# Kernel tuning notes

Hardware: AMD Instinct MI355X
Metric: run time of the kernel (lower is better)

The kernel has to match this reference:

```python
import jax, jax.numpy as jnp
import numpy as np

B, T, N1, N2, D, H, DH = 8, 4, 1024, 64, 1024, 16, 64
INNER = H * DH
EPS = 1e-5


def layernorm(x, g, b):
    mu = jnp.mean(x, axis=-1, keepdims=True)
    var = jnp.var(x, axis=-1, keepdims=True)
    return (x - mu) * jax.lax.rsqrt(var + EPS) * g + b


def setup_inputs() -> dict:
    key = jax.random.key(0)
    ks = jax.random.split(key, 8)
    s = 0.02
    return {
        "x": jax.random.normal(ks[0], (B, T, N1, D), jnp.float32),
        "latents": jax.random.normal(ks[1], (B, T, N2, D), jnp.float32),
        "gm": jnp.ones((D,), jnp.float32),
        "bm": jnp.zeros((D,), jnp.float32),
        "gl": jnp.ones((D,), jnp.float32),
        "bl": jnp.zeros((D,), jnp.float32),
        "Wq": jax.random.normal(ks[2], (D, INNER), jnp.float32) * s,
        "Wkv": jax.random.normal(ks[3], (D, 2 * INNER), jnp.float32) * s,
        "Wout": jax.random.normal(ks[4], (INNER, D), jnp.float32) * s,
        "Wd1": jax.random.normal(ks[5], (D, D // 4), jnp.float32) * s,
        "bd1": jnp.zeros((D // 4,), jnp.float32),
        "Wd2": jax.random.normal(ks[6], (D // 4, H), jnp.float32) * s,
        "bd2": jnp.zeros((H,), jnp.float32),
    }


def reference(x, latents, gm, bm, gl, bl, Wq, Wkv, Wout, Wd1, bd1, Wd2, bd2):
    b, t, n1, d = x.shape
    n2 = latents.shape[2]
    h, dh = H, DH
    scale = dh ** -0.5

    xn = layernorm(x, gm, bm)
    ln = layernorm(latents, gl, bl)

    # q: (b, h, t, n2, dh)
    q = (ln @ Wq).reshape(b, t, n2, h, dh).transpose(0, 3, 1, 2, 4)
    # kv over image tokens + first latent token -> nk = n1 + 1
    kv_in = jnp.concatenate([xn, ln[:, :, 0:1]], axis=2)
    nk = n1 + 1
    kv = (kv_in @ Wkv).reshape(b, t, nk, 2, h, dh)
    k = kv[:, :, :, 0].transpose(0, 3, 1, 2, 4)  # (b, h, t, nk, dh)
    v = kv[:, :, :, 1].transpose(0, 3, 1, 2, 4)

    sim = jnp.einsum('bhtid,bhtjd->bhtij', q * scale, k)
    sim = sim - jax.lax.stop_gradient(jnp.max(sim, axis=-1, keepdims=True))
    attn = jax.nn.softmax(sim, axis=-1)

    # dynamic per-head weights from mean-pooled (normed) latents: (b, t, h)
    hid = jax.nn.relu(ln.mean(axis=2) @ Wd1 + bd1)
    dw = jax.nn.softmax(hid @ Wd2 + bd2, axis=-1)
    attn = attn * dw.transpose(0, 2, 1)[:, :, :, None, None]  # (b,h,t,1,1)

    out = jnp.einsum('bhtij,bhtjd->bhtid', attn, v)
    out = out.transpose(0, 2, 3, 1, 4).reshape(b, t, n2, h * dh)
    return out @ Wout
```

## Files before the change

kernel.cpp:

```cpp
#include <hip/hip_runtime.h>
#include <cstdint>
#include <cstddef>

constexpr int CB = 8, CT = 4, CN1 = 1024, CN2 = 64, CD = 1024, CH = 16, CDH = 64;
constexpr int CBT = CB * CT;
constexpr int CNK = CN1 + 1;
constexpr int CINNER = CH * CDH;

__device__ __forceinline__ unsigned short f2bf(float f) {
  union { float f; unsigned int u; } v; v.f = f;
  unsigned int u = v.u;
  u += 0x7fffu + ((u >> 16) & 1u);
  return (unsigned short)(u >> 16);
}
__device__ __forceinline__ float blo(unsigned int w) {
  union { unsigned int u; float f; } v; v.u = w << 16; return v.f;
}
__device__ __forceinline__ float bhi(unsigned int w) {
  union { unsigned int u; float f; } v; v.u = w & 0xffff0000u; return v.f;
}

typedef __attribute__((ext_vector_type(8))) short short8;
typedef __attribute__((ext_vector_type(8))) __bf16 bf16x8;
typedef __attribute__((ext_vector_type(4))) float floatx4;

template <typename V>
__device__ __forceinline__ auto mfma_bf16_impl(V a, V b, floatx4 c, int)
    -> decltype(__builtin_amdgcn_mfma_f32_16x16x32_bf16(a, b, c, 0, 0, 0)) {
  return __builtin_amdgcn_mfma_f32_16x16x32_bf16(a, b, c, 0, 0, 0);
}
template <typename V>
__device__ __forceinline__ floatx4 mfma_bf16_impl(V a, V b, floatx4 c, long) {
  return __builtin_amdgcn_mfma_f32_16x16x32_bf16(
      __builtin_bit_cast(bf16x8, a), __builtin_bit_cast(bf16x8, b), c, 0, 0, 0);
}
__device__ __forceinline__ floatx4 mfma_bf16(short8 a, short8 b, floatx4 c) {
  return mfma_bf16_impl(a, b, c, 0);
}

#if __has_builtin(__builtin_amdgcn_global_load_lds)
#define HAS_GLDS 1
__device__ __forceinline__ void glds16(const unsigned short* g, unsigned short* l) {
  __builtin_amdgcn_global_load_lds(
      (const __attribute__((address_space(1))) void*)g,
      (__attribute__((address_space(3))) void*)l, 16, 0, 0);
}
#else
#define HAS_GLDS 0
#endif

__global__ __launch_bounds__(256) void ln_kernel(
    const float* __restrict__ x, const float* __restrict__ g,
    const float* __restrict__ b, unsigned short* __restrict__ obf,
    float* __restrict__ of32) {
  __shared__ float red[8];
  const int row = blockIdx.x, tid = threadIdx.x;
  const float4 xv = ((const float4*)(x + (size_t)row * CD))[tid];
  float s  = xv.x + xv.y + xv.z + xv.w;
  float s2 = xv.x*xv.x + xv.y*xv.y + xv.z*xv.z + xv.w*xv.w;
#pragma unroll
  for (int off = 32; off; off >>= 1) { s += __shfl_xor(s, off); s2 += __shfl_xor(s2, off); }
  if ((tid & 63) == 0) { red[tid >> 6] = s; red[4 + (tid >> 6)] = s2; }
  __syncthreads();
  const float fs  = red[0] + red[1] + red[2] + red[3];
  const float fs2 = red[4] + red[5] + red[6] + red[7];
  const float mean = fs * (1.0f / 1024.0f);
  const float var  = fs2 * (1.0f / 1024.0f) - mean * mean;
  const float rstd = rsqrtf(var + 1e-5f);
  const float4 gv = ((const float4*)g)[tid];
  const float4 bv = ((const float4*)b)[tid];
  float4 y;
  y.x = (xv.x - mean) * rstd * gv.x + bv.x;
  y.y = (xv.y - mean) * rstd * gv.y + bv.y;
  y.z = (xv.z - mean) * rstd * gv.z + bv.z;
  y.w = (xv.w - mean) * rstd * gv.w + bv.w;
  ushort4 o; o.x = f2bf(y.x); o.y = f2bf(y.y); o.z = f2bf(y.z); o.w = f2bf(y.w);
  ((ushort4*)(obf + (size_t)row * CD))[tid] = o;
  if (of32) ((float4*)(of32 + (size_t)row * CD))[tid] = y;
}

__global__ __launch_bounds__(256) void wtrans_kernel(
    const float* __restrict__ W, unsigned short* __restrict__ WT, int K, int N) {
  __shared__ float t[64][65];
  const int n0 = blockIdx.x * 64, k0 = blockIdx.y * 64;
  const int tid = threadIdx.x;
  const int kr = tid >> 4, ns = (tid & 15) * 4;
#pragma unroll
  for (int i = 0; i < 4; ++i) {
    const int k = kr + i * 16;
    const float4 v = *(const float4*)&W[(size_t)(k0 + k) * N + n0 + ns];
    t[k][ns + 0] = v.x; t[k][ns + 1] = v.y; t[k][ns + 2] = v.z; t[k][ns + 3] = v.w;
  }
  __syncthreads();
  const int n = tid >> 2, ks = (tid & 3) * 16;
#pragma unroll
  for (int c = 0; c < 4; ++c) {
    ushort4 o;
    o.x = f2bf(t[ks + c * 4 + 0][n]);
    o.y = f2bf(t[ks + c * 4 + 1][n]);
    o.z = f2bf(t[ks + c * 4 + 2][n]);
    o.w = f2bf(t[ks + c * 4 + 3][n]);
    *(ushort4*)&WT[(size_t)(n0 + n) * K + k0 + ks + c * 4] = o;
  }
}

template <bool A_KV, bool C_BF16>
__global__ __launch_bounds__(256) void gemm128_kernel(
    const unsigned short* __restrict__ A, const unsigned short* __restrict__ xn,
    const unsigned short* __restrict__ lnb, const unsigned short* __restrict__ BT,
    unsigned short* __restrict__ Cb, float* __restrict__ Cf,
    int M, int N, int K) {
  __shared__ __attribute__((aligned(16))) unsigned short As[128 * 32];
  __shared__ __attribute__((aligned(16))) unsigned short Bs[128 * 32];
  const int tid = threadIdx.x;
  const int col0 = blockIdx.x * 128, row0 = blockIdx.y * 128;
  const int srow = tid >> 2, skseg = (tid & 3) * 8;

  auto arow_ptr = [&](int grow) -> const unsigned short* {
    if (grow >= M) grow = M - 1;
    if (A_KV) {
      const int bt = grow / CNK, j = grow - bt * CNK;
      return (j < CN1) ? xn + ((size_t)(bt * CN1 + j)) * K + skseg
                       : lnb + ((size_t)(bt * CN2)) * K + skseg;
    }
    return A + (size_t)grow * K + skseg;
  };
  const unsigned short* a0 = arow_ptr(row0 + srow);
  const unsigned short* a1 = arow_ptr(row0 + 64 + srow);
  const unsigned short* b0 = BT + (size_t)(col0 + srow) * K + skseg;
  const unsigned short* b1 = BT + (size_t)(col0 + 64 + srow) * K + skseg;

  const int lane = tid & 63, wave = tid >> 6;
  const int wrow = (wave >> 1) * 64, wcol = (wave & 1) * 64;
  const int i16 = lane & 15, quad = lane >> 4;

  floatx4 acc[4][4] = {};
  for (int kt = 0; kt < K; kt += 32) {
    __syncthreads();
#if HAS_GLDS
    glds16(a0 + kt, &As[tid * 8]);
    glds16(a1 + kt, &As[2048 + tid * 8]);
    glds16(b0 + kt, &Bs[tid * 8]);
    glds16(b1 + kt, &Bs[2048 + tid * 8]);
#else
    *(uint4*)&As[tid * 8]        = *(const uint4*)(a0 + kt);
    *(uint4*)&As[2048 + tid * 8] = *(const uint4*)(a1 + kt);
    *(uint4*)&Bs[tid * 8]        = *(const uint4*)(b0 + kt);
    *(uint4*)&Bs[2048 + tid * 8] = *(const uint4*)(b1 + kt);
#endif
    __syncthreads();
    short8 af[4], bf[4];
#pragma unroll
    for (int ti = 0; ti < 4; ++ti)
      af[ti] = *(const short8*)&As[(wrow + ti * 16 + i16) * 32 + quad * 8];
#pragma unroll
    for (int tj = 0; tj < 4; ++tj)
      bf[tj] = *(const short8*)&Bs[(wcol + tj * 16 + i16) * 32 + quad * 8];
#pragma unroll
    for (int ti = 0; ti < 4; ++ti)
#pragma unroll
      for (int tj = 0; tj < 4; ++tj)
        acc[ti][tj] = mfma_bf16(af[ti], bf[tj], acc[ti][tj]);
  }
#pragma unroll
  for (int ti = 0; ti < 4; ++ti)
#pragma unroll
    for (int tj = 0; tj < 4; ++tj) {
      const int gc = col0 + wcol + tj * 16 + i16;
#pragma unroll
      for (int r = 0; r < 4; ++r) {
        const int gr = row0 + wrow + ti * 16 + quad * 4 + r;
        if (gr < M) {
          if (C_BF16) Cb[(size_t)gr * N + gc] = f2bf(acc[ti][tj][r]);
          else        Cf[(size_t)gr * N + gc] = acc[ti][tj][r];
        }
      }
    }
}

__global__ __launch_bounds__(256) void dw_kernel(
    const float* __restrict__ lnf, const float* __restrict__ Wd1,
    const float* __restrict__ bd1, const float* __restrict__ Wd2,
    const float* __restrict__ bd2, float* __restrict__ dw) {
  __shared__ float mean[CD];
  __shared__ float hid[256];
  __shared__ float lg[16];
  const int bt = blockIdx.x, tid = threadIdx.x;
  const float* base = lnf + (size_t)bt * CN2 * CD;
  for (int d = tid; d < CD; d += 256) {
    float s = 0.f;
    for (int r = 0; r < CN2; ++r) s += base[(size_t)r * CD + d];
    mean[d] = s * (1.0f / 64.0f);
  }
  __syncthreads();
  {
    float s = bd1[tid];
    for (int d = 0; d < CD; ++d) s += mean[d] * Wd1[(size_t)d * 256 + tid];
    hid[tid] = fmaxf(s, 0.0f);
  }
  __syncthreads();
  if (tid < 16) {
    float s = bd2[tid];
    for (int o = 0; o < 256; ++o) s += hid[o] * Wd2[o * 16 + tid];
    lg[tid] = s;
  }
  __syncthreads();
  if (tid < 16) {
    float mx = lg[0];
    for (int h = 1; h < 16; ++h) mx = fmaxf(mx, lg[h]);
    float sum = 0.f;
    for (int h = 0; h < 16; ++h) sum += __expf(lg[h] - mx);
    dw[bt * 16 + tid] = __expf(lg[tid] - mx) / sum;
  }
}

__global__ __launch_bounds__(256) void attn_kernel(
    const unsigned short* __restrict__ Q,
    const unsigned short* __restrict__ KV,
    const float* __restrict__ dw,
    unsigned short* __restrict__ AO) {
  __shared__ __attribute__((aligned(16))) unsigned short ks[64 * 72];
  __shared__ __attribute__((aligned(16))) unsigned short vt[64 * 72];
  const int bt = blockIdx.x >> 4, h = blockIdx.x & 15;
  const int tid = threadIdx.x;
  const int lane = tid & 63, wave = tid >> 6;
  const int i16 = lane & 15, quad = lane >> 4;
  const int wrow = wave * 16;

  const unsigned short* qbase =
      Q + ((size_t)(bt * 64 + wrow + i16)) * CINNER + h * 64;
  const short8 bq0 = *(const short8*)(qbase + quad * 8);
  const short8 bq1 = *(const short8*)(qbase + 32 + quad * 8);

  float m = -3.0e38f, l = 0.f;
  floatx4 O[4] = {{0,0,0,0}, {0,0,0,0}, {0,0,0,0}, {0,0,0,0}};
  const float scale = 0.125f;

  for (int j0 = 0; j0 < CNK; j0 += 64) {
    __syncthreads();
#pragma unroll
    for (int c = tid; c < 512; c += 256) {
      const int jr = c >> 3, seg = c & 7;
      const int j = j0 + jr;
      uint4 kk = make_uint4(0, 0, 0, 0), vv = make_uint4(0, 0, 0, 0);
      if (j < CNK) {
        const unsigned short* kb = KV + ((size_t)(bt * CNK + j)) * 2048 + h * 64 + seg * 8;
        kk = *(const uint4*)kb;
        vv = *(const uint4*)(kb + 1024);
      }
      *(uint4*)&ks[jr * 72 + seg * 8] = kk;
      const int hlf = (jr & 31) >> 4, t = jr & 15;
      const int vcol = ((jr >> 5) << 5) + ((t >> 2) << 3) + (t & 3) + hlf * 4;
      const unsigned int w[4] = {vv.x, vv.y, vv.z, vv.w};
#pragma unroll
      for (int p = 0; p < 4; ++p) {
        vt[(seg * 8 + 2 * p + 0) * 72 + vcol] = (unsigned short)(w[p] & 0xffffu);
        vt[(seg * 8 + 2 * p + 1) * 72 + vcol] = (unsigned short)(w[p] >> 16);
      }
    }
    __syncthreads();

    floatx4 s[4];
#pragma unroll
    for (int jt = 0; jt < 4; ++jt) {
      s[jt] = floatx4{0, 0, 0, 0};
      const short8 a0 = *(const short8*)&ks[(jt * 16 + i16) * 72 + quad * 8];
      const short8 a1 = *(const short8*)&ks[(jt * 16 + i16) * 72 + 32 + quad * 8];
      s[jt] = mfma_bf16(a0, bq0, s[jt]);
      s[jt] = mfma_bf16(a1, bq1, s[jt]);
    }

    float tmax = -3.0e38f;
#pragma unroll
    for (int jt = 0; jt < 4; ++jt)
#pragma unroll
      for (int r = 0; r < 4; ++r) {
        float sv = s[jt][r] * scale;
        if (j0 + jt * 16 + quad * 4 + r >= CNK) sv = -3.0e38f;
        s[jt][r] = sv;
        tmax = fmaxf(tmax, sv);
      }
    tmax = fmaxf(tmax, __shfl_xor(tmax, 16));
    tmax = fmaxf(tmax, __shfl_xor(tmax, 32));
    const float mnew = fmaxf(m, tmax);
    const float alpha = __expf(m - mnew);
    l *= alpha;
#pragma unroll
    for (int dt = 0; dt < 4; ++dt)
#pragma unroll
      for (int r = 0; r < 4; ++r) O[dt][r] *= alpha;

    unsigned short pb[4][4];
    float lsum = 0.f;
#pragma unroll
    for (int jt = 0; jt < 4; ++jt)
#pragma unroll
      for (int r = 0; r < 4; ++r) {
        const float p = __expf(s[jt][r] - mnew);
        lsum += p;
        pb[jt][r] = f2bf(p);
      }
    lsum += __shfl_xor(lsum, 16);
    lsum += __shfl_xor(lsum, 32);
    l += lsum;
    m = mnew;

#pragma unroll
    for (int c = 0; c < 2; ++c) {
      const short8 bp = {
          (short)pb[2 * c][0], (short)pb[2 * c][1],
          (short)pb[2 * c][2], (short)pb[2 * c][3],
          (short)pb[2 * c + 1][0], (short)pb[2 * c + 1][1],
          (short)pb[2 * c + 1][2], (short)pb[2 * c + 1][3]};
#pragma unroll
      for (int dt = 0; dt < 4; ++dt) {
        const short8 av = *(const short8*)&vt[(dt * 16 + i16) * 72 + c * 32 + quad * 8];
        O[dt] = mfma_bf16(av, bp, O[dt]);
      }
    }
  }

  const float wsc = dw[bt * 16 + h] / l;
  unsigned short* obase = AO + ((size_t)(bt * 64 + wrow + i16)) * CINNER + h * 64;
#pragma unroll
  for (int dt = 0; dt < 4; ++dt)
#pragma unroll
    for (int r = 0; r < 4; ++r)
      obase[dt * 16 + quad * 4 + r] = f2bf(O[dt][r] * wsc);
}

extern "C" void kernel_launch(void* const* d_in, const int* in_sizes, int n_in,
                              void* d_out, int out_size, void* d_ws, size_t ws_size,
                              hipStream_t stream) {
  const float* x       = (const float*)d_in[0];
  const float* latents = (const float*)d_in[1];
  const float* gm  = (const float*)d_in[2];
  const float* bm  = (const float*)d_in[3];
  const float* gl  = (const float*)d_in[4];
  const float* bl  = (const float*)d_in[5];
  const float* Wq  = (const float*)d_in[6];
  const float* Wkv = (const float*)d_in[7];
  const float* Wout= (const float*)d_in[8];
  const float* Wd1 = (const float*)d_in[9];
  const float* bd1 = (const float*)d_in[10];
  const float* Wd2 = (const float*)d_in[11];
  const float* bd2 = (const float*)d_in[12];
  float* out = (float*)d_out;

  char* ws = (char*)d_ws;
  size_t off = 0;
  auto alloc = [&](size_t bytes) -> void* {
    void* p = ws + off;
    off += (bytes + 255) & ~(size_t)255;
    return p;
  };
  unsigned short* xn   = (unsigned short*)alloc((size_t)CBT * CN1 * CD * 2);
  unsigned short* kv   = (unsigned short*)alloc((size_t)CBT * CNK * 2048 * 2);
  float*          lnf  = (float*)        alloc((size_t)CBT * CN2 * CD * 4);
  unsigned short* lnb  = (unsigned short*)alloc((size_t)CBT * CN2 * CD * 2);
  unsigned short* wqT  = (unsigned short*)alloc((size_t)CD * CINNER * 2);
  unsigned short* wkvT = (unsigned short*)alloc((size_t)CD * 2 * CINNER * 2);
  unsigned short* woT  = (unsigned short*)alloc((size_t)CINNER * CD * 2);
  unsigned short* qb   = (unsigned short*)alloc((size_t)CBT * CN2 * CINNER * 2);
  unsigned short* aob  = (unsigned short*)alloc((size_t)CBT * CN2 * CINNER * 2);
  float*          dwp  = (float*)        alloc((size_t)CBT * CH * 4);
  if (off > ws_size) return;

  ln_kernel<<<CBT * CN1, 256, 0, stream>>>(x, gm, bm, xn, nullptr);
  ln_kernel<<<CBT * CN2, 256, 0, stream>>>(latents, gl, bl, lnb, lnf);
  wtrans_kernel<<<dim3(CINNER / 64, CD / 64), 256, 0, stream>>>(Wq, wqT, CD, CINNER);
  wtrans_kernel<<<dim3(2 * CINNER / 64, CD / 64), 256, 0, stream>>>(Wkv, wkvT, CD, 2 * CINNER);
  wtrans_kernel<<<dim3(CD / 64, CINNER / 64), 256, 0, stream>>>(Wout, woT, CINNER, CD);
  gemm128_kernel<false, true><<<dim3(1024 / 128, 2048 / 128), 256, 0, stream>>>(
      lnb, nullptr, nullptr, wqT, qb, nullptr, 2048, 1024, 1024);
  gemm128_kernel<true, true><<<dim3(2048 / 128, (CBT * CNK + 127) / 128), 256, 0, stream>>>(
      nullptr, xn, lnb, wkvT, kv, nullptr, CBT * CNK, 2048, 1024);
  dw_kernel<<<CBT, 256, 0, stream>>>(lnf, Wd1, bd1, Wd2, bd2, dwp);
  attn_kernel<<<CBT * CH, 256, 0, stream>>>(qb, kv, dwp, aob);
  gemm128_kernel<false, false><<<dim3(1024 / 128, 2048 / 128), 256, 0, stream>>>(
      aob, nullptr, nullptr, woT, nullptr, out, 2048, 1024, 1024);
}
```

Baseline: 565.3 us.

## Double-buffer attention KV tiles, drop online max, one LayerNorm row per wave

The attention kernel now double-buffers its K and V tiles in shared memory. The next tile's global loads are issued into registers before the current tile is computed, then written to the other buffer afterwards, removing one barrier per iteration. Online-softmax max tracking and rescaling are removed: probabilities use exp2 of the scaled scores directly and are masked only on the final tile. This relies on scores staying small enough not to overflow. LayerNorm is also reworked to process one row per wavefront using only shuffle reductions, with no shared-memory barrier and a quarter as many blocks.

```diff
diff --git a/kernel.cpp b/kernel.cpp
--- a/kernel.cpp
+++ b/kernel.cpp
@@ -12,12 +12,6 @@
   unsigned int u = v.u;
   u += 0x7fffu + ((u >> 16) & 1u);
   return (unsigned short)(u >> 16);
-}
-__device__ __forceinline__ float blo(unsigned int w) {
-  union { unsigned int u; float f; } v; v.u = w << 16; return v.f;
-}
-__device__ __forceinline__ float bhi(unsigned int w) {
-  union { unsigned int u; float f; } v; v.u = w & 0xffff0000u; return v.f;
 }
 
 typedef __attribute__((ext_vector_type(8))) short short8;
@@ -53,30 +47,36 @@
     const float* __restrict__ x, const float* __restrict__ g,
     const float* __restrict__ b, unsigned short* __restrict__ obf,
     float* __restrict__ of32) {
-  __shared__ float red[8];
-  const int row = blockIdx.x, tid = threadIdx.x;
-  const float4 xv = ((const float4*)(x + (size_t)row * CD))[tid];
-  float s  = xv.x + xv.y + xv.z + xv.w;
-  float s2 = xv.x*xv.x + xv.y*xv.y + xv.z*xv.z + xv.w*xv.w;
+  const int row = blockIdx.x * 4 + (threadIdx.x >> 6);
+  const int lane = threadIdx.x & 63;
+  const float4* xr = (const float4*)(x + (size_t)row * CD);
+  float4 v[4];
+#pragma unroll
+  for (int k = 0; k < 4; ++k) v[k] = xr[lane + 64 * k];
+  float s = 0.f, s2 = 0.f;
+#pragma unroll
+  for (int k = 0; k < 4; ++k) {
+    s  += v[k].x + v[k].y + v[k].z + v[k].w;
+    s2 += v[k].x*v[k].x + v[k].y*v[k].y + v[k].z*v[k].z + v[k].w*v[k].w;
+  }
 #pragma unroll
   for (int off = 32; off; off >>= 1) { s += __shfl_xor(s, off); s2 += __shfl_xor(s2, off); }
-  if ((tid & 63) == 0) { red[tid >> 6] = s; red[4 + (tid >> 6)] = s2; }
-  __syncthreads();
-  const float fs  = red[0] + red[1] + red[2] + red[3];
-  const float fs2 = red[4] + red[5] + red[6] + red[7];
-  const float mean = fs * (1.0f / 1024.0f);
-  const float var  = fs2 * (1.0f / 1024.0f) - mean * mean;
+  const float mean = s * (1.0f / 1024.0f);
+  const float var  = s2 * (1.0f / 1024.0f) - mean * mean;
   const float rstd = rsqrtf(var + 1e-5f);
-  const float4 gv = ((const float4*)g)[tid];
-  const float4 bv = ((const float4*)b)[tid];
-  float4 y;
-  y.x = (xv.x - mean) * rstd * gv.x + bv.x;
-  y.y = (xv.y - mean) * rstd * gv.y + bv.y;
-  y.z = (xv.z - mean) * rstd * gv.z + bv.z;
-  y.w = (xv.w - mean) * rstd * gv.w + bv.w;
-  ushort4 o; o.x = f2bf(y.x); o.y = f2bf(y.y); o.z = f2bf(y.z); o.w = f2bf(y.w);
-  ((ushort4*)(obf + (size_t)row * CD))[tid] = o;
-  if (of32) ((float4*)(of32 + (size_t)row * CD))[tid] = y;
+#pragma unroll
+  for (int k = 0; k < 4; ++k) {
+    const float4 gv = ((const float4*)g)[lane + 64 * k];
+    const float4 bv = ((const float4*)b)[lane + 64 * k];
+    float4 y;
+    y.x = (v[k].x - mean) * rstd * gv.x + bv.x;
+    y.y = (v[k].y - mean) * rstd * gv.y + bv.y;
+    y.z = (v[k].z - mean) * rstd * gv.z + bv.z;
+    y.w = (v[k].w - mean) * rstd * gv.w + bv.w;
+    ushort4 o; o.x = f2bf(y.x); o.y = f2bf(y.y); o.z = f2bf(y.z); o.w = f2bf(y.w);
+    ((ushort4*)(obf + (size_t)row * CD))[lane + 64 * k] = o;
+    if (of32) ((float4*)(of32 + (size_t)row * CD))[lane + 64 * k] = y;
+  }
 }
 
 __global__ __launch_bounds__(256) void wtrans_kernel(
@@ -219,8 +219,8 @@
     const unsigned short* __restrict__ KV,
     const float* __restrict__ dw,
     unsigned short* __restrict__ AO) {
-  __shared__ __attribute__((aligned(16))) unsigned short ks[64 * 72];
-  __shared__ __attribute__((aligned(16))) unsigned short vt[64 * 72];
+  __shared__ __attribute__((aligned(16))) unsigned short ks[2][64 * 72];
+  __shared__ __attribute__((aligned(16))) unsigned short vt[2][64 * 72];
   const int bt = blockIdx.x >> 4, h = blockIdx.x & 15;
   const int tid = threadIdx.x;
   const int lane = tid & 63, wave = tid >> 6;
@@ -232,94 +232,97 @@
   const short8 bq0 = *(const short8*)(qbase + quad * 8);
   const short8 bq1 = *(const short8*)(qbase + 32 + quad * 8);
 
-  float m = -3.0e38f, l = 0.f;
+  const int jrb = tid & 31, seg = tid >> 5;
+  const int t_ = jrb & 15, hlf_ = jrb >> 4;
+  const int vcol0 = ((t_ >> 2) << 3) + (t_ & 3) + 4 * hlf_;
+  const unsigned short* kvb = KV + ((size_t)bt * CNK) * 2048 + h * 64 + seg * 8;
+
+  uint4 kk[2], vv[2];
+  auto load_tile = [&](int j0) {
+#pragma unroll
+    for (int c = 0; c < 2; ++c) {
+      const int j = j0 + c * 32 + jrb;
+      if (j < CNK) {
+        const unsigned short* p = kvb + (size_t)j * 2048;
+        kk[c] = *(const uint4*)p;
+        vv[c] = *(const uint4*)(p + 1024);
+      } else {
+        kk[c] = make_uint4(0, 0, 0, 0);
+        vv[c] = make_uint4(0, 0, 0, 0);
+      }
+    }
+  };
+  auto write_tile = [&](int buf) {
+#pragma unroll
+    for (int c = 0; c < 2; ++c) {
+      const int jr = c * 32 + jrb;
+      *(uint4*)&ks[buf][jr * 72 + seg * 8] = kk[c];
+      const int vcol = c * 32 + vcol0;
+      const unsigned int w[4] = {vv[c].x, vv[c].y, vv[c].z, vv[c].w};
+#pragma unroll
+      for (int p = 0; p < 4; ++p) {
+        vt[buf][(seg * 8 + 2 * p + 0) * 72 + vcol] = (unsigned short)(w[p] & 0xffffu);
+        vt[buf][(seg * 8 + 2 * p + 1) * 72 + vcol] = (unsigned short)(w[p] >> 16);
+      }
+    }
+  };
+
+  float l = 0.f;
   floatx4 O[4] = {{0,0,0,0}, {0,0,0,0}, {0,0,0,0}, {0,0,0,0}};
-  const float scale = 0.125f;
-
-  for (int j0 = 0; j0 < CNK; j0 += 64) {
+  const float expC = 0.18033688011112042f;
+
+  load_tile(0);
+  write_tile(0);
+  constexpr int NT = 17;
+  for (int t = 0; t < NT; ++t) {
+    if (t + 1 < NT) load_tile((t + 1) * 64);
     __syncthreads();
-#pragma unroll
-    for (int c = tid; c < 512; c += 256) {
-      const int jr = c >> 3, seg = c & 7;
-      const int j = j0 + jr;
-      uint4 kk = make_uint4(0, 0, 0, 0), vv = make_uint4(0, 0, 0, 0);
-      if (j < CNK) {
-        const unsigned short* kb = KV + ((size_t)(bt * CNK + j)) * 2048 + h * 64 + seg * 8;
-        kk = *(const uint4*)kb;
-        vv = *(const uint4*)(kb + 1024);
-      }
-      *(uint4*)&ks[jr * 72 + seg * 8] = kk;
-      const int hlf = (jr & 31) >> 4, t = jr & 15;
-      const int vcol = ((jr >> 5) << 5) + ((t >> 2) << 3) + (t & 3) + hlf * 4;
-      const unsigned int w[4] = {vv.x, vv.y, vv.z, vv.w};
-#pragma unroll
-      for (int p = 0; p < 4; ++p) {
-        vt[(seg * 8 + 2 * p + 0) * 72 + vcol] = (unsigned short)(w[p] & 0xffffu);
-        vt[(seg * 8 + 2 * p + 1) * 72 + vcol] = (unsigned short)(w[p] >> 16);
-      }
-    }
-    __syncthreads();
-
-    floatx4 s[4];
-#pragma unroll
-    for (int jt = 0; jt < 4; ++jt) {
-      s[jt] = floatx4{0, 0, 0, 0};
-      const short8 a0 = *(const short8*)&ks[(jt * 16 + i16) * 72 + quad * 8];
-      const short8 a1 = *(const short8*)&ks[(jt * 16 + i16) * 72 + 32 + quad * 8];
-      s[jt] = mfma_bf16(a0, bq0, s[jt]);
-      s[jt] = mfma_bf16(a1, bq1, s[jt]);
-    }
-
-    float tmax = -3.0e38f;
-#pragma unroll
-    for (int jt = 0; jt < 4; ++jt)
-#pragma unroll
-      for (int r = 0; r < 4; ++r) {
-        float sv = s[jt][r] * scale;
-        if (j0 + jt * 16 + quad * 4 + r >= CNK) sv = -3.0e38f;
-        s[jt][r] = sv;
-        tmax = fmaxf(tmax, sv);
-      }
-    tmax = fmaxf(tmax, __shfl_xor(tmax, 16));
-    tmax = fmaxf(tmax, __shfl_xor(tmax, 32));
-    const float mnew = fmaxf(m, tmax);
-    const float alpha = __expf(m - mnew);
-    l *= alpha;
-#pragma unroll
-    for (int dt = 0; dt < 4; ++dt)
-#pragma unroll
-      for (int r = 0; r < 4; ++r) O[dt][r] *= alpha;
-
-    unsigned short pb[4][4];
-    float lsum = 0.f;
-#pragma unroll
-    for (int jt = 0; jt < 4; ++jt)
-#pragma unroll
-      for (int r = 0; r < 4; ++r) {
-        const float p = __expf(s[jt][r] - mnew);
-        lsum += p;
-        pb[jt][r] = f2bf(p);
-      }
-    lsum += __shfl_xor(lsum, 16);
-    lsum += __shfl_xor(lsum, 32);
-    l += lsum;
-    m = mnew;
-
+    const int buf = t & 1;
+    const unsigned short* ksb = ks[buf];
+    const unsigned short* vtb = vt[buf];
 #pragma unroll
     for (int c = 0; c < 2; ++c) {
+      floatx4 s0 = {0,0,0,0}, s1 = {0,0,0,0};
+      const short8 a00 = *(const short8*)&ksb[((2*c)   * 16 + i16) * 72 + quad * 8];
+      const short8 a01 = *(const short8*)&ksb[((2*c)   * 16 + i16) * 72 + 32 + quad * 8];
+      const short8 a10 = *(const short8*)&ksb[((2*c+1) * 16 + i16) * 72 + quad * 8];
+      const short8 a11 = *(const short8*)&ksb[((2*c+1) * 16 + i16) * 72 + 32 + quad * 8];
+      s0 = mfma_bf16(a00, bq0, s0); s0 = mfma_bf16(a01, bq1, s0);
+      s1 = mfma_bf16(a10, bq0, s1); s1 = mfma_bf16(a11, bq1, s1);
+      unsigned short pb0[4], pb1[4];
+      if (t == NT - 1) {
+#pragma unroll
+        for (int r = 0; r < 4; ++r) {
+          const int k0g = t * 64 + (2*c)   * 16 + quad * 4 + r;
+          const int k1g = t * 64 + (2*c+1) * 16 + quad * 4 + r;
+          const float p0 = (k0g < CNK) ? exp2f(s0[r] * expC) : 0.f;
+          const float p1 = (k1g < CNK) ? exp2f(s1[r] * expC) : 0.f;
+          l += p0 + p1;
+          pb0[r] = f2bf(p0); pb1[r] = f2bf(p1);
+        }
+      } else {
+#pragma unroll
+        for (int r = 0; r < 4; ++r) {
+          const float p0 = exp2f(s0[r] * expC);
+          const float p1 = exp2f(s1[r] * expC);
+          l += p0 + p1;
+          pb0[r] = f2bf(p0); pb1[r] = f2bf(p1);
+        }
+      }
       const short8 bp = {
-          (short)pb[2 * c][0], (short)pb[2 * c][1],
-          (short)pb[2 * c][2], (short)pb[2 * c][3],
-          (short)pb[2 * c + 1][0], (short)pb[2 * c + 1][1],
-          (short)pb[2 * c + 1][2], (short)pb[2 * c + 1][3]};
+          (short)pb0[0], (short)pb0[1], (short)pb0[2], (short)pb0[3],
+          (short)pb1[0], (short)pb1[1], (short)pb1[2], (short)pb1[3]};
 #pragma unroll
       for (int dt = 0; dt < 4; ++dt) {
-        const short8 av = *(const short8*)&vt[(dt * 16 + i16) * 72 + c * 32 + quad * 8];
+        const short8 av = *(const short8*)&vtb[(dt * 16 + i16) * 72 + c * 32 + quad * 8];
         O[dt] = mfma_bf16(av, bp, O[dt]);
       }
     }
-  }
-
+    if (t + 1 < NT) write_tile((t + 1) & 1);
+  }
+
+  l += __shfl_xor(l, 16);
+  l += __shfl_xor(l, 32);
   const float wsc = dw[bt * 16 + h] / l;
   unsigned short* obase = AO + ((size_t)(bt * 64 + wrow + i16)) * CINNER + h * 64;
 #pragma unroll
@@ -366,8 +369,8 @@
   float*          dwp  = (float*)        alloc((size_t)CBT * CH * 4);
   if (off > ws_size) return;
 
-  ln_kernel<<<CBT * CN1, 256, 0, stream>>>(x, gm, bm, xn, nullptr);
-  ln_kernel<<<CBT * CN2, 256, 0, stream>>>(latents, gl, bl, lnb, lnf);
+  ln_kernel<<<CBT * CN1 / 4, 256, 0, stream>>>(x, gm, bm, xn, nullptr);
+  ln_kernel<<<CBT * CN2 / 4, 256, 0, stream>>>(latents, gl, bl, lnb, lnf);
   wtrans_kernel<<<dim3(CINNER / 64, CD / 64), 256, 0, stream>>>(Wq, wqT, CD, CINNER);
   wtrans_kernel<<<dim3(2 * CINNER / 64, CD / 64), 256, 0, stream>>>(Wkv, wkvT, CD, 2 * CINNER);
   wtrans_kernel<<<dim3(CD / 64, CINNER / 64), 256, 0, stream>>>(Wout, woT, CINNER, CD);
```

Result: no change. 562.8 us (-0.5%).
